# Kernel optimization log

Measured on AMD Instinct MI355X. Metric: run time of the kernel, lower is better.

## Reference

```python
import jax, jax.numpy as jnp
import numpy as np

HEADS = 8
DIM_HEAD = 64
SCALE = DIM_HEAD ** -0.5


def setup_inputs() -> dict:
    key = jax.random.key(0)
    k1, k2, k3, k4 = jax.random.split(key, 4)
    b, dim, l = 4, 512, 2048
    hidden = HEADS * DIM_HEAD  # 512
    x = jax.random.normal(k1, (b, dim, l), dtype=jnp.float32)
    w_qkv = jax.random.normal(k2, (3 * hidden, dim), dtype=jnp.float32) * (dim ** -0.5)
    w_out = jax.random.normal(k3, (dim, hidden), dtype=jnp.float32) * (hidden ** -0.5)
    b_out = jax.random.normal(k4, (dim,), dtype=jnp.float32) * 0.01
    return {"x": x, "w_qkv": w_qkv, "w_out": w_out, "b_out": b_out}


def reference(x, w_qkv, w_out, b_out):
    b, c, l = x.shape
    h, d = HEADS, DIM_HEAD
    # 1x1 Conv1d == channel matmul: [3*hidden, c] x [b, c, l] -> [b, 3*hidden, l]
    qkv = jnp.einsum('oc,bcl->bol', w_qkv, x)
    q, k, v = jnp.split(qkv, 3, axis=1)
    # 'b (h d) l -> b h d l'
    q = q.reshape(b, h, d, l) * SCALE
    k = k.reshape(b, h, d, l)
    v = v.reshape(b, h, d, l)
    sim = jnp.einsum('bhdi,bhdj->bhij', q, k)          # [b, h, l, l]
    attn = jax.nn.softmax(sim, axis=-1)
    out = jnp.einsum('bhij,bhdj->bhid', attn, v)       # [b, h, l, d]
    # 'b h l d -> b (h d) l'
    out = out.transpose(0, 1, 3, 2).reshape(b, h * d, l)
    return jnp.einsum('oc,bcl->bol', w_out, out) + b_out[None, :, None]
```

## Files before the change

kernel.cpp:

```cpp
#include <hip/hip_runtime.h>

#define L_SEQ 2048
#define KDIM  512

typedef __attribute__((ext_vector_type(8))) short short8v;
typedef __attribute__((ext_vector_type(4))) float f32x4;

static __device__ __forceinline__ short f2b(float f) {
    union { float f; unsigned u; } v; v.f = f;
    unsigned r = v.u + 0x7fffu + ((v.u >> 16) & 1u);
    return (short)(r >> 16);
}

__global__ __launch_bounds__(256) void conv_w(
    const float* __restrict__ wq, const float* __restrict__ wo,
    short* __restrict__ wqb, short* __restrict__ wob)
{
    const int i = blockIdx.x * 256 + threadIdx.x;
    const int NQ = 1536 * 512 / 4;
    float4 v;
    if (i < NQ) v = ((const float4*)wq)[i];
    else        v = ((const float4*)wo)[i - NQ];
    short4 s;
    s.x = f2b(v.x); s.y = f2b(v.y); s.z = f2b(v.z); s.w = f2b(v.w);
    if (i < NQ) ((short4*)wqb)[i] = s;
    else        ((short4*)wob)[i - NQ] = s;
}

__global__ __launch_bounds__(256) void transpose_x(
    const float* __restrict__ x, short* __restrict__ xT)
{
    const int b  = blockIdx.z;
    const int c0 = blockIdx.y * 64;
    const int l0 = blockIdx.x * 64;
    __shared__ __align__(16) float T[64 * 72];
    const int t = threadIdx.x;

#pragma unroll
    for (int j = 0; j < 4; ++j) {
        const int idx = j * 256 + t;
        const int row = idx >> 4, c4 = idx & 15;
        const float4 v = *(const float4*)&x[((size_t)b * KDIM + c0 + row) * L_SEQ + l0 + c4 * 4];
        *(float4*)&T[row * 72 + c4 * 4] = v;
    }
    __syncthreads();

#pragma unroll
    for (int j = 0; j < 2; ++j) {
        const int idx = j * 256 + t;
        const int l = idx >> 3, ch = idx & 7;
        short8v s;
#pragma unroll
        for (int e = 0; e < 8; ++e)
            s[e] = f2b(T[(ch * 8 + e) * 72 + l]);
        *(short8v*)&xT[((size_t)b * L_SEQ + l0 + l) * KDIM + c0 + ch * 8] = s;
    }
}

template<int EPI>
__global__ __launch_bounds__(256) void gemm_bt(
    const short* __restrict__ Ag, const short* __restrict__ Bbase,
    const float* __restrict__ bias,
    short* __restrict__ Qws, short* __restrict__ Kws, short* __restrict__ Vws,
    float* __restrict__ Cout)
{
    const int bz = blockIdx.z;
    const int o0 = blockIdx.y * 128;
    const int l0 = blockIdx.x * 128;
    const short* Bg = Bbase + (size_t)bz * L_SEQ * KDIM;

    __shared__ __align__(16) char smem[2 * 128 * 72 * 2];
    short* sA = (short*)smem;
    short* sB = (short*)(smem + 128 * 72 * 2);

    const int t    = threadIdx.x;
    const int w    = t >> 6;
    const int lane = t & 63;
    const int quad = lane >> 4;
    const int l16  = lane & 15;
    const int wo   = (w & 1) * 64;
    const int wl   = (w >> 1) * 64;

    f32x4 acc[4][4];
#pragma unroll
    for (int i = 0; i < 4; ++i)
#pragma unroll
        for (int n = 0; n < 4; ++n) acc[i][n] = (f32x4){0,0,0,0};

    for (int k0 = 0; k0 < KDIM; k0 += 64) {
#pragma unroll
        for (int j = 0; j < 4; ++j) {
            const int idx = j * 256 + t;
            const int r = idx >> 3, c = idx & 7;
            *(float4*)&sA[r * 72 + c * 8] =
                *(const float4*)&Ag[(size_t)(o0 + r) * KDIM + k0 + c * 8];
            *(float4*)&sB[r * 72 + c * 8] =
                *(const float4*)&Bg[(size_t)(l0 + r) * KDIM + k0 + c * 8];
        }
        __syncthreads();

#pragma unroll
        for (int ks = 0; ks < 2; ++ks) {
            short8v af[4], bf[4];
#pragma unroll
            for (int i = 0; i < 4; ++i)
                af[i] = *(const short8v*)&sA[(wo + i * 16 + l16) * 72 + ks * 32 + quad * 8];
#pragma unroll
            for (int n = 0; n < 4; ++n)
                bf[n] = *(const short8v*)&sB[(wl + n * 16 + l16) * 72 + ks * 32 + quad * 8];
#pragma unroll
            for (int i = 0; i < 4; ++i)
#pragma unroll
                for (int n = 0; n < 4; ++n)
                    acc[i][n] = __builtin_amdgcn_mfma_f32_16x16x32_bf16(af[i], bf[n], acc[i][n], 0, 0, 0);
        }
        __syncthreads();
    }

    if (EPI == 0) {
        const int type  = o0 >> 9;
        const int local = o0 & 511;
        const int bh0   = bz * 8 + (local >> 6);
        const float sc  = (type == 0) ? 0.125f : 1.0f;
        short* T = sA;

        if (type == 2) {
#pragma unroll
            for (int i = 0; i < 4; ++i)
#pragma unroll
                for (int n = 0; n < 4; ++n)
#pragma unroll
                    for (int r = 0; r < 4; ++r)
                        T[(wo + i * 16 + quad * 4 + r) * 136 + wl + n * 16 + l16] =
                            f2b(acc[i][n][r]);
            __syncthreads();
#pragma unroll
            for (int p = 0; p < 8; ++p) {
                const int idx = p * 256 + t;
                const int o = idx >> 4, c = idx & 15;
                const float4 v = *(const float4*)&T[o * 136 + c * 8];
                short* dst = Vws + ((size_t)(bh0 + (o >> 6)) * 64 + (o & 63)) * L_SEQ + l0 + c * 8;
                *(float4*)dst = v;
            }
        } else {
#pragma unroll
            for (int i = 0; i < 4; ++i)
#pragma unroll
                for (int n = 0; n < 4; ++n) {
                    short4 s;
                    s.x = f2b(acc[i][n][0] * sc);
                    s.y = f2b(acc[i][n][1] * sc);
                    s.z = f2b(acc[i][n][2] * sc);
                    s.w = f2b(acc[i][n][3] * sc);
                    *(short4*)&T[(wl + n * 16 + l16) * 136 + wo + i * 16 + quad * 4] = s;
                }
            __syncthreads();
            short* base = (type == 0) ? Qws : Kws;
#pragma unroll
            for (int p = 0; p < 8; ++p) {
                const int idx = p * 256 + t;
                const int l = idx >> 4, c = idx & 15;
                const float4 v = *(const float4*)&T[l * 136 + c * 8];
                short* dst = base + ((size_t)(bh0 + (c >> 3)) * L_SEQ + l0 + l) * 64 + (c & 7) * 8;
                *(float4*)dst = v;
            }
        }
    } else {
        float* Cb = Cout + (size_t)bz * KDIM * L_SEQ;
#pragma unroll
        for (int i = 0; i < 4; ++i) {
            const int o = o0 + wo + i * 16 + quad * 4;
            float bv[4];
#pragma unroll
            for (int r = 0; r < 4; ++r) bv[r] = bias[o + r];
#pragma unroll
            for (int n = 0; n < 4; ++n) {
                const int l = l0 + wl + n * 16 + l16;
#pragma unroll
                for (int r = 0; r < 4; ++r)
                    Cb[(size_t)(o + r) * L_SEQ + l] = acc[i][n][r] + bv[r];
            }
        }
    }
}

__global__ __launch_bounds__(256) void attn_mfma(
    const short* __restrict__ Qws, const short* __restrict__ Kws,
    const short* __restrict__ Vws, short* __restrict__ ao)
{
    const int b  = blockIdx.z;
    const int h  = blockIdx.y;
    const int i0 = blockIdx.x * 64;
    const int bh = b * 8 + h;

    __shared__ __align__(16) char smem[27648];
    short* Kld = (short*)smem;
    short* Vld = (short*)(smem + 9216);
    short* Pld = (short*)(smem + 18432);
    float* Old = (float*)smem;

    const int t    = threadIdx.x;
    const int w    = t >> 6;
    const int lane = t & 63;
    const int quad = lane >> 4;
    const int l16  = lane & 15;

    const short* Qb = Qws + (size_t)bh * L_SEQ * 64;
    const short* Kb = Kws + (size_t)bh * L_SEQ * 64;
    const short* Vb = Vws + (size_t)bh * 64 * L_SEQ;

    short8v qa0, qa1;
    {
        const short* qrow = Qb + (size_t)(i0 + w * 16 + l16) * 64 + quad * 8;
        qa0 = *(const short8v*)qrow;
        qa1 = *(const short8v*)(qrow + 32);
    }

    f32x4 oacc[4] = {{0,0,0,0},{0,0,0,0},{0,0,0,0},{0,0,0,0}};
    float rsum[4] = {0.f, 0.f, 0.f, 0.f};
    short* Pw = Pld + w * 16 * 72;

    for (int j0 = 0; j0 < L_SEQ; j0 += 64) {
        {
            const int r = t >> 2, c = t & 3;
            const float4 k0 = *(const float4*)(Kb + (size_t)(j0 + r) * 64 + c * 16);
            const float4 k1 = *(const float4*)(Kb + (size_t)(j0 + r) * 64 + c * 16 + 8);
            const float4 v0 = *(const float4*)(Vb + (size_t)r * L_SEQ + j0 + c * 16);
            const float4 v1 = *(const float4*)(Vb + (size_t)r * L_SEQ + j0 + c * 16 + 8);
            *(float4*)&Kld[r * 72 + c * 16]     = k0;
            *(float4*)&Kld[r * 72 + c * 16 + 8] = k1;
            *(float4*)&Vld[r * 72 + c * 16]     = v0;
            *(float4*)&Vld[r * 72 + c * 16 + 8] = v1;
        }
        __syncthreads();

        f32x4 sacc[4] = {{0,0,0,0},{0,0,0,0},{0,0,0,0},{0,0,0,0}};
#pragma unroll
        for (int n = 0; n < 4; ++n) {
            short8v kf0 = *(const short8v*)&Kld[(n * 16 + l16) * 72 + quad * 8];
            short8v kf1 = *(const short8v*)&Kld[(n * 16 + l16) * 72 + 32 + quad * 8];
            sacc[n] = __builtin_amdgcn_mfma_f32_16x16x32_bf16(qa0, kf0, sacc[n], 0, 0, 0);
            sacc[n] = __builtin_amdgcn_mfma_f32_16x16x32_bf16(qa1, kf1, sacc[n], 0, 0, 0);
        }

#pragma unroll
        for (int n = 0; n < 4; ++n)
#pragma unroll
            for (int r = 0; r < 4; ++r) {
                const float p = __expf(sacc[n][r]);
                rsum[r] += p;
                Pw[(quad * 4 + r) * 72 + n * 16 + l16] = f2b(p);
            }

        short8v pa0 = *(const short8v*)&Pw[l16 * 72 + quad * 8];
        short8v pa1 = *(const short8v*)&Pw[l16 * 72 + 32 + quad * 8];
#pragma unroll
        for (int n = 0; n < 4; ++n) {
            short8v vf0 = *(const short8v*)&Vld[(n * 16 + l16) * 72 + quad * 8];
            short8v vf1 = *(const short8v*)&Vld[(n * 16 + l16) * 72 + 32 + quad * 8];
            oacc[n] = __builtin_amdgcn_mfma_f32_16x16x32_bf16(pa0, vf0, oacc[n], 0, 0, 0);
            oacc[n] = __builtin_amdgcn_mfma_f32_16x16x32_bf16(pa1, vf1, oacc[n], 0, 0, 0);
        }
        __syncthreads();
    }

#pragma unroll
    for (int r = 0; r < 4; ++r) {
#pragma unroll
        for (int m = 1; m < 16; m <<= 1)
            rsum[r] += __shfl_xor(rsum[r], m, 64);
        rsum[r] = 1.0f / rsum[r];
    }

#pragma unroll
    for (int n = 0; n < 4; ++n)
#pragma unroll
        for (int r = 0; r < 4; ++r)
            Old[(w * 16 + quad * 4 + r) * 68 + n * 16 + l16] = oacc[n][r] * rsum[r];
    __syncthreads();
#pragma unroll
    for (int p = 0; p < 4; ++p) {
        const int idx = p * 256 + t;
        const int i = idx >> 4, c4 = idx & 15;
        const float4 v = *(const float4*)&Old[i * 68 + c4 * 4];
        short4 s;
        s.x = f2b(v.x); s.y = f2b(v.y); s.z = f2b(v.z); s.w = f2b(v.w);
        *(short4*)&ao[((size_t)b * L_SEQ + i0 + i) * KDIM + h * 64 + c4 * 4] = s;
    }
}

extern "C" void kernel_launch(void* const* d_in, const int* in_sizes, int n_in,
                              void* d_out, int out_size, void* d_ws, size_t ws_size,
                              hipStream_t stream)
{
    const float* x     = (const float*)d_in[0];
    const float* w_qkv = (const float*)d_in[1];
    const float* w_out = (const float*)d_in[2];
    const float* b_out = (const float*)d_in[3];
    float* out = (float*)d_out;

    char* ws = (char*)d_ws;
    short* xT    = (short*)ws;                      ws += (size_t)4 * L_SEQ * KDIM * 2;
    short* wq_bf = (short*)ws;                      ws += (size_t)1536 * 512 * 2;
    short* wo_bf = (short*)ws;                      ws += (size_t)512 * 512 * 2;
    short* Qws   = (short*)ws;                      ws += (size_t)32 * L_SEQ * 64 * 2;
    short* Kws   = (short*)ws;                      ws += (size_t)32 * L_SEQ * 64 * 2;
    short* Vws   = (short*)ws;                      ws += (size_t)32 * L_SEQ * 64 * 2;
    short* ao    = (short*)ws;

    dim3 blk(256);
    conv_w     <<<dim3(1024), blk, 0, stream>>>(w_qkv, w_out, wq_bf, wo_bf);
    transpose_x<<<dim3(32, 8, 4), blk, 0, stream>>>(x, xT);
    gemm_bt<0> <<<dim3(16, 12, 4), blk, 0, stream>>>(wq_bf, xT, nullptr, Qws, Kws, Vws, nullptr);
    attn_mfma  <<<dim3(32, 8, 4), blk, 0, stream>>>(Qws, Kws, Vws, ao);
    gemm_bt<1> <<<dim3(16, 4, 4), blk, 0, stream>>>(wo_bf, ao, b_out, nullptr, nullptr, nullptr, out);
}
```

Before: 182.0 us.

## Double attention query tile per block and fold log2e into Q scale for exp2

Each attention block now handles 128 query rows instead of 64. Each wave holds two 16-row query sub-tiles, so every K/V tile staged in shared memory is reused twice as much and global K/V traffic is halved. The Q scale now includes log2(e), which lets the softmax numerator use the hardware exp2 instruction directly instead of __expf. In exchange the kernel uses more registers and shared memory and launches half as many blocks (512), which may lower occupancy. The softmax still has no max subtraction, as before.

```diff
diff --git a/kernel.cpp b/kernel.cpp
--- a/kernel.cpp
+++ b/kernel.cpp
@@ -10,6 +10,14 @@
     union { float f; unsigned u; } v; v.f = f;
     unsigned r = v.u + 0x7fffu + ((v.u >> 16) & 1u);
     return (short)(r >> 16);
+}
+
+static __device__ __forceinline__ float fast_exp2(float x) {
+#if __has_builtin(__builtin_amdgcn_exp2f)
+    return __builtin_amdgcn_exp2f(x);
+#else
+    return exp2f(x);
+#endif
 }
 
 __global__ __launch_bounds__(256) void conv_w(
@@ -121,7 +129,7 @@
         const int type  = o0 >> 9;
         const int local = o0 & 511;
         const int bh0   = bz * 8 + (local >> 6);
-        const float sc  = (type == 0) ? 0.125f : 1.0f;
+        const float sc  = (type == 0) ? 0.18033688011112042f : 1.0f;
         short* T = sA;
 
         if (type == 2) {
@@ -190,10 +198,10 @@
 {
     const int b  = blockIdx.z;
     const int h  = blockIdx.y;
-    const int i0 = blockIdx.x * 64;
+    const int i0 = blockIdx.x * 128;
     const int bh = b * 8 + h;
 
-    __shared__ __align__(16) char smem[27648];
+    __shared__ __align__(16) char smem[36864];
     short* Kld = (short*)smem;
     short* Vld = (short*)(smem + 9216);
     short* Pld = (short*)(smem + 18432);
@@ -209,16 +217,21 @@
     const short* Kb = Kws + (size_t)bh * L_SEQ * 64;
     const short* Vb = Vws + (size_t)bh * 64 * L_SEQ;
 
-    short8v qa0, qa1;
-    {
-        const short* qrow = Qb + (size_t)(i0 + w * 16 + l16) * 64 + quad * 8;
-        qa0 = *(const short8v*)qrow;
-        qa1 = *(const short8v*)(qrow + 32);
-    }
-
-    f32x4 oacc[4] = {{0,0,0,0},{0,0,0,0},{0,0,0,0},{0,0,0,0}};
-    float rsum[4] = {0.f, 0.f, 0.f, 0.f};
-    short* Pw = Pld + w * 16 * 72;
+    short8v qa[2][2];
+#pragma unroll
+    for (int hh = 0; hh < 2; ++hh) {
+        const short* qrow = Qb + (size_t)(i0 + w * 32 + hh * 16 + l16) * 64 + quad * 8;
+        qa[hh][0] = *(const short8v*)qrow;
+        qa[hh][1] = *(const short8v*)(qrow + 32);
+    }
+
+    f32x4 oacc[2][4];
+#pragma unroll
+    for (int hh = 0; hh < 2; ++hh)
+#pragma unroll
+        for (int n = 0; n < 4; ++n) oacc[hh][n] = (f32x4){0,0,0,0};
+    float rsum[2][4] = {{0,0,0,0},{0,0,0,0}};
+    short* Pw = Pld + w * 32 * 72;
 
     for (int j0 = 0; j0 < L_SEQ; j0 += 64) {
         {
@@ -234,52 +247,73 @@
         }
         __syncthreads();
 
-        f32x4 sacc[4] = {{0,0,0,0},{0,0,0,0},{0,0,0,0},{0,0,0,0}};
+        f32x4 sacc[2][4];
+#pragma unroll
+        for (int hh = 0; hh < 2; ++hh)
+#pragma unroll
+            for (int n = 0; n < 4; ++n) sacc[hh][n] = (f32x4){0,0,0,0};
 #pragma unroll
         for (int n = 0; n < 4; ++n) {
             short8v kf0 = *(const short8v*)&Kld[(n * 16 + l16) * 72 + quad * 8];
             short8v kf1 = *(const short8v*)&Kld[(n * 16 + l16) * 72 + 32 + quad * 8];
-            sacc[n] = __builtin_amdgcn_mfma_f32_16x16x32_bf16(qa0, kf0, sacc[n], 0, 0, 0);
-            sacc[n] = __builtin_amdgcn_mfma_f32_16x16x32_bf16(qa1, kf1, sacc[n], 0, 0, 0);
-        }
-
-#pragma unroll
-        for (int n = 0; n < 4; ++n)
-#pragma unroll
-            for (int r = 0; r < 4; ++r) {
-                const float p = __expf(sacc[n][r]);
-                rsum[r] += p;
-                Pw[(quad * 4 + r) * 72 + n * 16 + l16] = f2b(p);
-            }
-
-        short8v pa0 = *(const short8v*)&Pw[l16 * 72 + quad * 8];
-        short8v pa1 = *(const short8v*)&Pw[l16 * 72 + 32 + quad * 8];
+#pragma unroll
+            for (int hh = 0; hh < 2; ++hh) {
+                sacc[hh][n] = __builtin_amdgcn_mfma_f32_16x16x32_bf16(qa[hh][0], kf0, sacc[hh][n], 0, 0, 0);
+                sacc[hh][n] = __builtin_amdgcn_mfma_f32_16x16x32_bf16(qa[hh][1], kf1, sacc[hh][n], 0, 0, 0);
+            }
+        }
+
+#pragma unroll
+        for (int hh = 0; hh < 2; ++hh)
+#pragma unroll
+            for (int n = 0; n < 4; ++n)
+#pragma unroll
+                for (int r = 0; r < 4; ++r) {
+                    const float p = fast_exp2(sacc[hh][n][r]);
+                    rsum[hh][r] += p;
+                    Pw[(hh * 16 + quad * 4 + r) * 72 + n * 16 + l16] = f2b(p);
+                }
+
+        short8v pa[2][2];
+#pragma unroll
+        for (int hh = 0; hh < 2; ++hh) {
+            pa[hh][0] = *(const short8v*)&Pw[(hh * 16 + l16) * 72 + quad * 8];
+            pa[hh][1] = *(const short8v*)&Pw[(hh * 16 + l16) * 72 + 32 + quad * 8];
+        }
 #pragma unroll
         for (int n = 0; n < 4; ++n) {
             short8v vf0 = *(const short8v*)&Vld[(n * 16 + l16) * 72 + quad * 8];
             short8v vf1 = *(const short8v*)&Vld[(n * 16 + l16) * 72 + 32 + quad * 8];
-            oacc[n] = __builtin_amdgcn_mfma_f32_16x16x32_bf16(pa0, vf0, oacc[n], 0, 0, 0);
-            oacc[n] = __builtin_amdgcn_mfma_f32_16x16x32_bf16(pa1, vf1, oacc[n], 0, 0, 0);
+#pragma unroll
+            for (int hh = 0; hh < 2; ++hh) {
+                oacc[hh][n] = __builtin_amdgcn_mfma_f32_16x16x32_bf16(pa[hh][0], vf0, oacc[hh][n], 0, 0, 0);
+                oacc[hh][n] = __builtin_amdgcn_mfma_f32_16x16x32_bf16(pa[hh][1], vf1, oacc[hh][n], 0, 0, 0);
+            }
         }
         __syncthreads();
     }
 
 #pragma unroll
-    for (int r = 0; r < 4; ++r) {
-#pragma unroll
-        for (int m = 1; m < 16; m <<= 1)
-            rsum[r] += __shfl_xor(rsum[r], m, 64);
-        rsum[r] = 1.0f / rsum[r];
-    }
-
-#pragma unroll
-    for (int n = 0; n < 4; ++n)
-#pragma unroll
-        for (int r = 0; r < 4; ++r)
-            Old[(w * 16 + quad * 4 + r) * 68 + n * 16 + l16] = oacc[n][r] * rsum[r];
+    for (int hh = 0; hh < 2; ++hh)
+#pragma unroll
+        for (int r = 0; r < 4; ++r) {
+#pragma unroll
+            for (int m = 1; m < 16; m <<= 1)
+                rsum[hh][r] += __shfl_xor(rsum[hh][r], m, 64);
+            rsum[hh][r] = 1.0f / rsum[hh][r];
+        }
+
+#pragma unroll
+    for (int hh = 0; hh < 2; ++hh)
+#pragma unroll
+        for (int n = 0; n < 4; ++n)
+#pragma unroll
+            for (int r = 0; r < 4; ++r)
+                Old[(w * 32 + hh * 16 + quad * 4 + r) * 68 + n * 16 + l16] =
+                    oacc[hh][n][r] * rsum[hh][r];
     __syncthreads();
 #pragma unroll
-    for (int p = 0; p < 4; ++p) {
+    for (int p = 0; p < 8; ++p) {
         const int idx = p * 256 + t;
         const int i = idx >> 4, c4 = idx & 15;
         const float4 v = *(const float4*)&Old[i * 68 + c4 * 4];
@@ -312,6 +346,6 @@
     conv_w     <<<dim3(1024), blk, 0, stream>>>(w_qkv, w_out, wq_bf, wo_bf);
     transpose_x<<<dim3(32, 8, 4), blk, 0, stream>>>(x, xT);
     gemm_bt<0> <<<dim3(16, 12, 4), blk, 0, stream>>>(wq_bf, xT, nullptr, Qws, Kws, Vws, nullptr);
-    attn_mfma  <<<dim3(32, 8, 4), blk, 0, stream>>>(Qws, Kws, Vws, ao);
+    attn_mfma  <<<dim3(16, 8, 4), blk, 0, stream>>>(Qws, Kws, Vws, ao);
     gemm_bt<1> <<<dim3(16, 4, 4), blk, 0, stream>>>(wo_bf, ao, b_out, nullptr, nullptr, nullptr, out);
 }
```

Result: no change. 179.3 us (-1.5%).
